# Kernel optimization log

Measured on AMD Instinct MI355X. Metric: run time of the kernel, lower is better.

## Reference

```python
import jax, jax.numpy as jnp
import numpy as np
from jax import lax

WINDOW = 11
C1 = 0.01 ** 2
C2 = 0.03 ** 2


def _box_sum_1d(x, k, axis):
    # sum over a length-k window along `axis`, zero-padded by k//2 (matches
    # torch avg_pool3d count_include_pad=True after dividing by k**3).
    window = [1] * x.ndim
    window[axis] = k
    pad = [(0, 0)] * x.ndim
    pad[axis] = (k // 2, k // 2)
    return lax.reduce_window(x, jnp.array(0.0, x.dtype), lax.add,
                             tuple(window), (1,) * x.ndim, pad)


def avg_pool3d(x, k=WINDOW):
    # separable box filter: O(3k) per voxel instead of O(k^3)
    s = _box_sum_1d(x, k, 2)
    s = _box_sum_1d(s, k, 3)
    s = _box_sum_1d(s, k, 4)
    return s / (k ** 3)


def ssim_loss_3d(pred, target):
    mu_p = avg_pool3d(pred)
    mu_t = avg_pool3d(target)
    mu_p_sq = mu_p ** 2
    mu_t_sq = mu_t ** 2
    mu_pt = mu_p * mu_t
    sigma_p = avg_pool3d(pred ** 2) - mu_p_sq
    sigma_t = avg_pool3d(target ** 2) - mu_t_sq
    sigma_pt = avg_pool3d(pred * target) - mu_pt
    ssim = ((2 * mu_pt + C1) * (2 * sigma_pt + C2)
            / ((mu_p_sq + mu_t_sq + C1) * (sigma_p + sigma_t + C2)))
    return 1.0 - ssim.mean()


def setup_inputs() -> dict:
    key = jax.random.key(0)
    k1, k2 = jax.random.split(key)
    shape = (4, 1, 128, 128, 128)  # [B, C, D, H, W]
    pred = jax.random.uniform(k1, shape, dtype=jnp.float32)
    target = jax.random.uniform(k2, shape, dtype=jnp.float32)
    return {"pred": pred, "target": target}


def reference(pred, target):
    l1_weight = 1.0
    ssim_weight = 0.5
    l1_loss = jnp.mean(jnp.abs(pred - target))
    ssim_loss = ssim_loss_3d(pred, target)
    total_loss = l1_weight * l1_loss + ssim_weight * ssim_loss
    reg_loss = jnp.array(0.0, dtype=total_loss.dtype)  # aux_info is None
    return total_loss, l1_loss, ssim_loss, reg_loss
```

## Files before the change

### kernel.cpp

```cpp
#include <hip/hip_runtime.h>
#include <hip/hip_fp16.h>


#define NB 4
#define ND 128
#define NH 128
#define NW 128
#define PLANE (NH * NW)
#define VOL (ND * PLANE)
#define VOL4 (NB * VOL)
#define K1_BLOCKS (NB * ND * 8)
#define K2_BLOCKS 1024
#define HS_F16 142

typedef _Float16 half2v __attribute__((ext_vector_type(2)));
typedef float f32x2 __attribute__((ext_vector_type(2)));

__global__ __launch_bounds__(256, 4) void k_wh(const float* __restrict__ p,
                                               const float* __restrict__ t,
                                               _Float16* __restrict__ S5,
                                               float* __restrict__ l1p)
{
    __shared__ _Float16 hs[4][16][HS_F16];
    __shared__ float red4[4];

    const int bid   = blockIdx.x;
    const int htile = bid & 7;
    const int d     = (bid >> 3) & 127;
    const int b     = bid >> 10;
    const int h0    = htile * 16;
    const int tid   = threadIdx.x;

    const int wp = tid & 63;
    const int c  = tid >> 6;
    const int hbase = h0 + c * 4;
    const int pbase = ((b * ND + d) * NH) * NW + 2 * wp;
    const int wcol  = 2 * wp + 6;

    const f32x2 z2 = {0.f, 0.f};

    f32x2 P[14], T[14];
#pragma unroll
    for (int i = 0; i < 14; ++i) {
        const int h = hbase - 5 + i;
        f32x2 pv = z2, tv = z2;
        if (h >= 0 && h < NH) {
            pv = *(const f32x2*)&p[pbase + h * NW];
            tv = *(const f32x2*)&t[pbase + h * NW];
        }
        P[i] = pv; T[i] = tv;
    }
    __builtin_amdgcn_sched_barrier(0);

    for (int idx = tid; idx < 4 * 16 * 14; idx += 256) {
        const int f = idx / 224;
        const int rem = idx - f * 224;
        const int r = rem / 14;
        const int c14 = rem - r * 14;
        const int col = (c14 < 6) ? c14 : (128 + c14);
        hs[f][r][col] = (_Float16)0.f;
    }
    __builtin_amdgcn_sched_barrier(0);

    f32x2 A_[14], D_[14];
#pragma unroll
    for (int i = 0; i < 14; ++i) {
        A_[i] = P[i] + T[i];
        D_[i] = P[i] - T[i];
    }

    float l1x = 0.f, l1y = 0.f;
#pragma unroll
    for (int i = 5; i <= 8; ++i) {
        l1x += fabsf(D_[i].x);
        l1y += fabsf(D_[i].y);
    }

    f32x2 sA = z2, sD = z2, sU = z2, sV = z2;
#pragma unroll
    for (int i = 0; i < 11; ++i) {
        const f32x2 a = A_[i], dd = D_[i];
        sA += a; sD += dd;
        sU += a * a; sV += dd * dd;
    }

#define STORE4(r) do {                                                        \
        half2v o_;                                                            \
        o_[0] = (_Float16)sA.x; o_[1] = (_Float16)sA.y;                       \
        *(half2v*)&hs[0][(r)][wcol] = o_;                                     \
        o_[0] = (_Float16)sD.x; o_[1] = (_Float16)sD.y;                       \
        *(half2v*)&hs[1][(r)][wcol] = o_;                                     \
        o_[0] = (_Float16)sU.x; o_[1] = (_Float16)sU.y;                       \
        *(half2v*)&hs[2][(r)][wcol] = o_;                                     \
        o_[0] = (_Float16)sV.x; o_[1] = (_Float16)sV.y;                       \
        *(half2v*)&hs[3][(r)][wcol] = o_;                                     \
    } while (0)

    STORE4(c * 4);
#pragma unroll
    for (int k = 1; k < 4; ++k) {
        const f32x2 an = A_[10 + k], dn = D_[10 + k];
        const f32x2 ao = A_[k - 1],  do_ = D_[k - 1];
        sA += an - ao;
        sD += dn - do_;
        sU += an * an - ao * ao;
        sV += dn * dn - do_ * do_;
        STORE4(c * 4 + k);
    }
#undef STORE4

    {
        float v = l1x + l1y;
#pragma unroll
        for (int off = 32; off > 0; off >>= 1) v += __shfl_down(v, off, 64);
        if ((tid & 63) == 0) red4[tid >> 6] = v;
    }
    __syncthreads();
    if (tid == 0) l1p[bid] = red4[0] + red4[1] + red4[2] + red4[3];

    const int ho = tid >> 4;
    const int wc = tid & 15;
    const size_t obase = (size_t)((b * ND + d) * NH + (h0 + ho)) * NW + wc * 8;

#pragma unroll
    for (int f = 0; f < 4; ++f) {
        half2v pr[10];
#pragma unroll
        for (int m = 0; m < 10; ++m)
            pr[m] = *(const half2v*)&hs[f][ho][8 * wc + 2 * m];
        float v[18];
#pragma unroll
        for (int k = 0; k < 18; ++k)
            v[k] = (k & 1) ? (float)pr[(k + 1) >> 1][0] : (float)pr[k >> 1][1];
        float s = 0.f;
#pragma unroll
        for (int j = 0; j < 11; ++j) s += v[j];
        union { _Float16 h8[8]; uint4 u; } o;
        o.h8[0] = (_Float16)s;
#pragma unroll
        for (int n = 1; n < 8; ++n) {
            s += v[10 + n] - v[n - 1];
            o.h8[n] = (_Float16)s;
        }
        *(uint4*)&S5[(size_t)f * VOL4 + obase] = o.u;
    }
}

__global__ __launch_bounds__(256) void k_d_ssim(const _Float16* __restrict__ S5,
                                                float* __restrict__ ssimp)
{
    __shared__ float red4[4];
    const float INV  = 1.0f / 1331.0f;
    const float INV2 = 1.0f / 2662.0f;
    const float C1f = 1e-4f, C2f = 9e-4f;

    const int bid = blockIdx.x;
    const int dc  = bid & 7;
    const int tid = threadIdx.x;
    const int idx = ((bid >> 3) << 8) + tid;
    const int wp = idx & 63;
    const int h  = (idx >> 6) & 127;
    const int b  = idx >> 13;
    const int d0 = dc * 16;
    const size_t base0 = (size_t)b * VOL + h * NW + wp * 2;

    const _Float16* F0 = S5 + 0 * (size_t)VOL4 + base0;
    const _Float16* F1 = S5 + 1 * (size_t)VOL4 + base0;
    const _Float16* F2 = S5 + 2 * (size_t)VOL4 + base0;
    const _Float16* F3 = S5 + 3 * (size_t)VOL4 + base0;

#define LOADF(F, dd) (*(const half2v*)&(F)[(size_t)(dd) * PLANE])

    half2v ring[4][11];
    float rsx[4] = {0.f, 0.f, 0.f, 0.f};
    float rsy[4] = {0.f, 0.f, 0.f, 0.f};

#pragma unroll
    for (int o = -5; o <= 5; ++o) {
        const int dd = d0 + o;
        half2v v0, v1, v2, v3;
        if (dd >= 0 && dd < ND) {
            v0 = LOADF(F0, dd); v1 = LOADF(F1, dd);
            v2 = LOADF(F2, dd); v3 = LOADF(F3, dd);
        } else {
            v0 = v1 = v2 = v3 = (half2v)(_Float16)0.f;
        }
        ring[0][o + 5] = v0; ring[1][o + 5] = v1;
        ring[2][o + 5] = v2; ring[3][o + 5] = v3;
        rsx[0] += (float)v0[0]; rsy[0] += (float)v0[1];
        rsx[1] += (float)v1[0]; rsy[1] += (float)v1[1];
        rsx[2] += (float)v2[0]; rsy[2] += (float)v2[1];
        rsx[3] += (float)v3[0]; rsy[3] += (float)v3[1];
    }

    float acc = 0.f;
#pragma unroll
    for (int s = 0; s < 16; ++s) {
        {
            const float muA = rsx[0] * INV, muD = rsx[1] * INV;
            const float mAA = muA * muA, mDD = muD * muD;
            const float P2 = 0.5f * (mAA - mDD);
            const float S2 = 0.5f * (mAA + mDD);
            const float num = (P2 + C1f) * fmaf(rsx[2] - rsx[3], INV2, C2f - P2);
            const float den = (S2 + C1f) * fmaf(rsx[2] + rsx[3], INV2, C2f - S2);
            acc = fmaf(num, __builtin_amdgcn_rcpf(den), acc);
        }
        {
            const float muA = rsy[0] * INV, muD = rsy[1] * INV;
            const float mAA = muA * muA, mDD = muD * muD;
            const float P2 = 0.5f * (mAA - mDD);
            const float S2 = 0.5f * (mAA + mDD);
            const float num = (P2 + C1f) * fmaf(rsy[2] - rsy[3], INV2, C2f - P2);
            const float den = (S2 + C1f) * fmaf(rsy[2] + rsy[3], INV2, C2f - S2);
            acc = fmaf(num, __builtin_amdgcn_rcpf(den), acc);
        }

        if (s < 15) {
            const int slot = s % 11;
            const int da = d0 + 6 + s;
            half2v n0, n1, n2, n3;
            if (da < ND) {
                n0 = LOADF(F0, da); n1 = LOADF(F1, da);
                n2 = LOADF(F2, da); n3 = LOADF(F3, da);
            } else {
                n0 = n1 = n2 = n3 = (half2v)(_Float16)0.f;
            }
            rsx[0] += (float)n0[0] - (float)ring[0][slot][0];
            rsy[0] += (float)n0[1] - (float)ring[0][slot][1];
            rsx[1] += (float)n1[0] - (float)ring[1][slot][0];
            rsy[1] += (float)n1[1] - (float)ring[1][slot][1];
            rsx[2] += (float)n2[0] - (float)ring[2][slot][0];
            rsy[2] += (float)n2[1] - (float)ring[2][slot][1];
            rsx[3] += (float)n3[0] - (float)ring[3][slot][0];
            rsy[3] += (float)n3[1] - (float)ring[3][slot][1];
            ring[0][slot] = n0; ring[1][slot] = n1;
            ring[2][slot] = n2; ring[3][slot] = n3;
        }
    }
#undef LOADF

    float v = acc;
#pragma unroll
    for (int off = 32; off > 0; off >>= 1) v += __shfl_down(v, off, 64);
    if ((tid & 63) == 0) red4[tid >> 6] = v;
    __syncthreads();
    if (tid == 0) ssimp[bid] = red4[0] + red4[1] + red4[2] + red4[3];
}

__global__ __launch_bounds__(256) void k_final(const float* __restrict__ l1p,
                                               const float* __restrict__ sp,
                                               float* __restrict__ out)
{
    __shared__ double r1[256];
    __shared__ double r2[256];
    const int tid = threadIdx.x;
    double s1 = 0.0, s2 = 0.0;
    for (int i = tid; i < K1_BLOCKS; i += 256) s1 += (double)l1p[i];
    for (int i = tid; i < K2_BLOCKS; i += 256) s2 += (double)sp[i];
    r1[tid] = s1; r2[tid] = s2;
    __syncthreads();
    for (int s = 128; s > 0; s >>= 1) {
        if (tid < s) { r1[tid] += r1[tid + s]; r2[tid] += r2[tid + s]; }
        __syncthreads();
    }
    if (tid == 0) {
        const double N = (double)VOL4;
        const double l1        = r1[0] / N;
        const double ssim_mean = r2[0] / N;
        const double ssim_loss = 1.0 - ssim_mean;
        out[0] = (float)(l1 + 0.5 * ssim_loss);
        out[1] = (float)l1;
        out[2] = (float)ssim_loss;
        out[3] = 0.f;
    }
}

extern "C" void kernel_launch(void* const* d_in, const int* in_sizes, int n_in,
                              void* d_out, int out_size, void* d_ws, size_t ws_size,
                              hipStream_t stream)
{
    const float* pred = (const float*)d_in[0];
    const float* targ = (const float*)d_in[1];
    float* out = (float*)d_out;

    _Float16* S5 = (_Float16*)d_ws;
    float* l1p   = (float*)((char*)d_ws + (size_t)4 * VOL4 * 2);
    float* ssimp = l1p + K1_BLOCKS;

    k_wh<<<K1_BLOCKS, 256, 0, stream>>>(pred, targ, S5, l1p);
    k_d_ssim<<<K2_BLOCKS, 256, 0, stream>>>(S5, ssimp);
    k_final<<<1, 256, 0, stream>>>(l1p, ssimp, out);
}
```

Before: 57.14 us.

## Interleave fp16 intermediates in pairs and enlarge H tile per block

The four fp16 partial-sum planes are regrouped into two buffers where each pair of fields is interleaved. This lets the depth pass fetch 8-byte vectors from two streams instead of four 4-byte streams. The first kernel now covers 32 rows per block with 8 rows per thread, which reduces halo reloads of pred/target, and it streams loads through a sliding window instead of preloading 14 rows. Costs are more LDS per block (lower occupancy) and half as many blocks.

```diff
diff --git a/kernel.cpp b/kernel.cpp
--- a/kernel.cpp
+++ b/kernel.cpp
@@ -9,79 +9,66 @@
 #define PLANE (NH * NW)
 #define VOL (ND * PLANE)
 #define VOL4 (NB * VOL)
-#define K1_BLOCKS (NB * ND * 8)
+#define K1_BLOCKS (NB * ND * 4)
 #define K2_BLOCKS 1024
 #define HS_F16 142
 
 typedef _Float16 half2v __attribute__((ext_vector_type(2)));
+typedef _Float16 half4v __attribute__((ext_vector_type(4)));
 typedef float f32x2 __attribute__((ext_vector_type(2)));
 
-__global__ __launch_bounds__(256, 4) void k_wh(const float* __restrict__ p,
-                                               const float* __restrict__ t,
-                                               _Float16* __restrict__ S5,
-                                               float* __restrict__ l1p)
-{
-    __shared__ _Float16 hs[4][16][HS_F16];
+__global__ __launch_bounds__(256) void k_wh(const float* __restrict__ p,
+                                            const float* __restrict__ t,
+                                            _Float16* __restrict__ G0,
+                                            _Float16* __restrict__ G1,
+                                            float* __restrict__ l1p)
+{
+    __shared__ _Float16 hs[4][32][HS_F16];
     __shared__ float red4[4];
 
     const int bid   = blockIdx.x;
-    const int htile = bid & 7;
-    const int d     = (bid >> 3) & 127;
-    const int b     = bid >> 10;
-    const int h0    = htile * 16;
+    const int htile = bid & 3;
+    const int d     = (bid >> 2) & 127;
+    const int b     = bid >> 9;
+    const int h0    = htile * 32;
     const int tid   = threadIdx.x;
 
-    const int wp = tid & 63;
-    const int c  = tid >> 6;
-    const int hbase = h0 + c * 4;
-    const int pbase = ((b * ND + d) * NH) * NW + 2 * wp;
-    const int wcol  = 2 * wp + 6;
-
-    const f32x2 z2 = {0.f, 0.f};
-
-    f32x2 P[14], T[14];
-#pragma unroll
-    for (int i = 0; i < 14; ++i) {
-        const int h = hbase - 5 + i;
-        f32x2 pv = z2, tv = z2;
-        if (h >= 0 && h < NH) {
-            pv = *(const f32x2*)&p[pbase + h * NW];
-            tv = *(const f32x2*)&t[pbase + h * NW];
-        }
-        P[i] = pv; T[i] = tv;
-    }
-    __builtin_amdgcn_sched_barrier(0);
-
-    for (int idx = tid; idx < 4 * 16 * 14; idx += 256) {
-        const int f = idx / 224;
-        const int rem = idx - f * 224;
+    for (int idx = tid; idx < 4 * 32 * 14; idx += 256) {
+        const int f = idx / 448;
+        const int rem = idx - f * 448;
         const int r = rem / 14;
         const int c14 = rem - r * 14;
         const int col = (c14 < 6) ? c14 : (128 + c14);
         hs[f][r][col] = (_Float16)0.f;
     }
-    __builtin_amdgcn_sched_barrier(0);
-
-    f32x2 A_[14], D_[14];
-#pragma unroll
-    for (int i = 0; i < 14; ++i) {
-        A_[i] = P[i] + T[i];
-        D_[i] = P[i] - T[i];
-    }
-
+
+    const int wp = tid & 63;
+    const int c  = tid >> 6;
+    const int hbase = h0 + c * 8;
+    const int pbase = ((b * ND + d) * NH) * NW + 2 * wp;
+    const int wcol  = 2 * wp + 6;
+
+    const f32x2 z2 = {0.f, 0.f};
+    f32x2 Aw[11], Dw[11];
+    f32x2 sA = z2, sD = z2, sU = z2, sV = z2;
     float l1x = 0.f, l1y = 0.f;
-#pragma unroll
-    for (int i = 5; i <= 8; ++i) {
-        l1x += fabsf(D_[i].x);
-        l1y += fabsf(D_[i].y);
-    }
-
-    f32x2 sA = z2, sD = z2, sU = z2, sV = z2;
+
 #pragma unroll
     for (int i = 0; i < 11; ++i) {
-        const f32x2 a = A_[i], dd = D_[i];
+        const int h = hbase - 5 + i;
+        f32x2 pv = z2, tv = z2;
+        if (h >= 0) {
+            pv = *(const f32x2*)&p[pbase + h * NW];
+            tv = *(const f32x2*)&t[pbase + h * NW];
+        }
+        const f32x2 a = pv + tv, dd = pv - tv;
+        Aw[i] = a; Dw[i] = dd;
         sA += a; sD += dd;
         sU += a * a; sV += dd * dd;
+        if (i >= 5) {
+            l1x += fabsf(dd.x);
+            l1y += fabsf(dd.y);
+        }
     }
 
 #define STORE4(r) do {                                                        \
@@ -96,16 +83,26 @@
         *(half2v*)&hs[3][(r)][wcol] = o_;                                     \
     } while (0)
 
-    STORE4(c * 4);
-#pragma unroll
-    for (int k = 1; k < 4; ++k) {
-        const f32x2 an = A_[10 + k], dn = D_[10 + k];
-        const f32x2 ao = A_[k - 1],  do_ = D_[k - 1];
-        sA += an - ao;
-        sD += dn - do_;
-        sU += an * an - ao * ao;
-        sV += dn * dn - do_ * do_;
-        STORE4(c * 4 + k);
+    STORE4(c * 8);
+#pragma unroll
+    for (int k = 1; k < 8; ++k) {
+        const int h = hbase + 5 + k;
+        f32x2 pv = z2, tv = z2;
+        if (h < NH) {
+            pv = *(const f32x2*)&p[pbase + h * NW];
+            tv = *(const f32x2*)&t[pbase + h * NW];
+        }
+        const f32x2 a = pv + tv, dd = pv - tv;
+        if (k <= 2) {
+            l1x += fabsf(dd.x);
+            l1y += fabsf(dd.y);
+        }
+        const f32x2 ao = Aw[k - 1], do_ = Dw[k - 1];
+        sA += a - ao;
+        sD += dd - do_;
+        sU += a * a - ao * ao;
+        sV += dd * dd - do_ * do_;
+        STORE4(c * 8 + k);
     }
 #undef STORE4
 
@@ -120,33 +117,43 @@
 
     const int ho = tid >> 4;
     const int wc = tid & 15;
-    const size_t obase = (size_t)((b * ND + d) * NH + (h0 + ho)) * NW + wc * 8;
-
-#pragma unroll
-    for (int f = 0; f < 4; ++f) {
-        half2v pr[10];
-#pragma unroll
-        for (int m = 0; m < 10; ++m)
-            pr[m] = *(const half2v*)&hs[f][ho][8 * wc + 2 * m];
-        float v[18];
-#pragma unroll
-        for (int k = 0; k < 18; ++k)
-            v[k] = (k & 1) ? (float)pr[(k + 1) >> 1][0] : (float)pr[k >> 1][1];
-        float s = 0.f;
-#pragma unroll
-        for (int j = 0; j < 11; ++j) s += v[j];
-        union { _Float16 h8[8]; uint4 u; } o;
-        o.h8[0] = (_Float16)s;
-#pragma unroll
-        for (int n = 1; n < 8; ++n) {
-            s += v[10 + n] - v[n - 1];
-            o.h8[n] = (_Float16)s;
-        }
-        *(uint4*)&S5[(size_t)f * VOL4 + obase] = o.u;
-    }
-}
-
-__global__ __launch_bounds__(256) void k_d_ssim(const _Float16* __restrict__ S5,
+
+#pragma unroll
+    for (int it = 0; it < 2; ++it) {
+        const int row = ho + 16 * it;
+        const size_t obase =
+            (size_t)((b * ND + d) * NH + (h0 + row)) * NW + wc * 8;
+
+#pragma unroll
+        for (int gp = 0; gp < 2; ++gp) {
+            float vA[18], vB[18];
+#pragma unroll
+            for (int m = 0; m < 10; ++m) {
+                const half2v ha = *(const half2v*)&hs[2 * gp][row][8 * wc + 2 * m];
+                const half2v hb = *(const half2v*)&hs[2 * gp + 1][row][8 * wc + 2 * m];
+                if (m > 0) { vA[2 * m - 1] = (float)ha[0]; vB[2 * m - 1] = (float)hb[0]; }
+                if (m < 9) { vA[2 * m]     = (float)ha[1]; vB[2 * m]     = (float)hb[1]; }
+            }
+            float sa = 0.f, sb = 0.f;
+#pragma unroll
+            for (int j = 0; j < 11; ++j) { sa += vA[j]; sb += vB[j]; }
+            union { _Float16 g[16]; uint4 q[2]; } o;
+            o.g[0] = (_Float16)sa; o.g[1] = (_Float16)sb;
+#pragma unroll
+            for (int n = 1; n < 8; ++n) {
+                sa += vA[10 + n] - vA[n - 1];
+                sb += vB[10 + n] - vB[n - 1];
+                o.g[2 * n] = (_Float16)sa; o.g[2 * n + 1] = (_Float16)sb;
+            }
+            _Float16* G = gp ? G1 : G0;
+            *(uint4*)&G[2 * obase]     = o.q[0];
+            *(uint4*)&G[2 * obase + 8] = o.q[1];
+        }
+    }
+}
+
+__global__ __launch_bounds__(256) void k_d_ssim(const _Float16* __restrict__ G0,
+                                                const _Float16* __restrict__ G1,
                                                 float* __restrict__ ssimp)
 {
     __shared__ float red4[4];
@@ -164,33 +171,26 @@
     const int d0 = dc * 16;
     const size_t base0 = (size_t)b * VOL + h * NW + wp * 2;
 
-    const _Float16* F0 = S5 + 0 * (size_t)VOL4 + base0;
-    const _Float16* F1 = S5 + 1 * (size_t)VOL4 + base0;
-    const _Float16* F2 = S5 + 2 * (size_t)VOL4 + base0;
-    const _Float16* F3 = S5 + 3 * (size_t)VOL4 + base0;
-
-#define LOADF(F, dd) (*(const half2v*)&(F)[(size_t)(dd) * PLANE])
-
-    half2v ring[4][11];
+#define LOADG(G, dd) (*(const half4v*)&(G)[2 * ((size_t)base0 + (size_t)(dd) * PLANE)])
+
+    half4v ring0[11], ring1[11];
     float rsx[4] = {0.f, 0.f, 0.f, 0.f};
     float rsy[4] = {0.f, 0.f, 0.f, 0.f};
 
 #pragma unroll
     for (int o = -5; o <= 5; ++o) {
         const int dd = d0 + o;
-        half2v v0, v1, v2, v3;
+        half4v g0, g1;
         if (dd >= 0 && dd < ND) {
-            v0 = LOADF(F0, dd); v1 = LOADF(F1, dd);
-            v2 = LOADF(F2, dd); v3 = LOADF(F3, dd);
+            g0 = LOADG(G0, dd); g1 = LOADG(G1, dd);
         } else {
-            v0 = v1 = v2 = v3 = (half2v)(_Float16)0.f;
-        }
-        ring[0][o + 5] = v0; ring[1][o + 5] = v1;
-        ring[2][o + 5] = v2; ring[3][o + 5] = v3;
-        rsx[0] += (float)v0[0]; rsy[0] += (float)v0[1];
-        rsx[1] += (float)v1[0]; rsy[1] += (float)v1[1];
-        rsx[2] += (float)v2[0]; rsy[2] += (float)v2[1];
-        rsx[3] += (float)v3[0]; rsy[3] += (float)v3[1];
+            g0 = g1 = (half4v)(_Float16)0.f;
+        }
+        ring0[o + 5] = g0; ring1[o + 5] = g1;
+        rsx[0] += (float)g0[0]; rsx[1] += (float)g0[1];
+        rsy[0] += (float)g0[2]; rsy[1] += (float)g0[3];
+        rsx[2] += (float)g1[0]; rsx[3] += (float)g1[1];
+        rsy[2] += (float)g1[2]; rsy[3] += (float)g1[3];
     }
 
     float acc = 0.f;
@@ -218,26 +218,25 @@
         if (s < 15) {
             const int slot = s % 11;
             const int da = d0 + 6 + s;
-            half2v n0, n1, n2, n3;
+            half4v n0, n1;
             if (da < ND) {
-                n0 = LOADF(F0, da); n1 = LOADF(F1, da);
-                n2 = LOADF(F2, da); n3 = LOADF(F3, da);
+                n0 = LOADG(G0, da); n1 = LOADG(G1, da);
             } else {
-                n0 = n1 = n2 = n3 = (half2v)(_Float16)0.f;
+                n0 = n1 = (half4v)(_Float16)0.f;
             }
-            rsx[0] += (float)n0[0] - (float)ring[0][slot][0];
-            rsy[0] += (float)n0[1] - (float)ring[0][slot][1];
-            rsx[1] += (float)n1[0] - (float)ring[1][slot][0];
-            rsy[1] += (float)n1[1] - (float)ring[1][slot][1];
-            rsx[2] += (float)n2[0] - (float)ring[2][slot][0];
-            rsy[2] += (float)n2[1] - (float)ring[2][slot][1];
-            rsx[3] += (float)n3[0] - (float)ring[3][slot][0];
-            rsy[3] += (float)n3[1] - (float)ring[3][slot][1];
-            ring[0][slot] = n0; ring[1][slot] = n1;
-            ring[2][slot] = n2; ring[3][slot] = n3;
-        }
-    }
-#undef LOADF
+            const half4v r0 = ring0[slot], r1 = ring1[slot];
+            rsx[0] += (float)n0[0] - (float)r0[0];
+            rsx[1] += (float)n0[1] - (float)r0[1];
+            rsy[0] += (float)n0[2] - (float)r0[2];
+            rsy[1] += (float)n0[3] - (float)r0[3];
+            rsx[2] += (float)n1[0] - (float)r1[0];
+            rsx[3] += (float)n1[1] - (float)r1[1];
+            rsy[2] += (float)n1[2] - (float)r1[2];
+            rsy[3] += (float)n1[3] - (float)r1[3];
+            ring0[slot] = n0; ring1[slot] = n1;
+        }
+    }
+#undef LOADG
 
     float v = acc;
 #pragma unroll
@@ -283,11 +282,12 @@
     const float* targ = (const float*)d_in[1];
     float* out = (float*)d_out;
 
-    _Float16* S5 = (_Float16*)d_ws;
-    float* l1p   = (float*)((char*)d_ws + (size_t)4 * VOL4 * 2);
+    _Float16* G0 = (_Float16*)d_ws;
+    _Float16* G1 = G0 + 2 * (size_t)VOL4;
+    float* l1p   = (float*)((char*)d_ws + (size_t)8 * VOL4);
     float* ssimp = l1p + K1_BLOCKS;
 
-    k_wh<<<K1_BLOCKS, 256, 0, stream>>>(pred, targ, S5, l1p);
-    k_d_ssim<<<K2_BLOCKS, 256, 0, stream>>>(S5, ssimp);
+    k_wh<<<K1_BLOCKS, 256, 0, stream>>>(pred, targ, G0, G1, l1p);
+    k_d_ssim<<<K2_BLOCKS, 256, 0, stream>>>(G0, G1, ssimp);
     k_final<<<1, 256, 0, stream>>>(l1p, ssimp, out);
 }
```

After: 63.99 us. 12.0% more time.
